# Kernel optimization log

Hardware: AMD Instinct MI355X
Metric: run time of the kernel (lower is better)

The kernel has to match this reference:

```python
import jax, jax.numpy as jnp
import numpy as np

B, Lc, Le, H, V = 128, 512, 512, 512, 128
PAD_IDX = 0  # ignore_index for cross entropy


def _lstm_cell(x, h, c, Wih, Whh, bih, bhh):
    # PyTorch gate order: i, f, g, o
    gates = x @ Wih.T + h @ Whh.T + bih + bhh
    i, f, g, o = jnp.split(gates, 4, axis=-1)
    c_new = jax.nn.sigmoid(f) * c + jax.nn.sigmoid(i) * jnp.tanh(g)
    h_new = jax.nn.sigmoid(o) * jnp.tanh(c_new)
    return h_new, c_new


def setup_inputs() -> dict:
    key = jax.random.key(0)
    ks = jax.random.split(key, 16)
    s = 0.05  # weight init scale
    inp = {
        "C": jax.random.normal(ks[0], (B, Lc, V), jnp.float32),
        "C_pad": jax.random.randint(ks[1], (B, Lc), 0, 2, jnp.int32).at[:, 0].set(0),
        "E": jax.random.randint(ks[2], (B, Le), 0, V, jnp.int32),
        "E_emb": jax.random.normal(ks[3], (B, Le, V), jnp.float32),
        # encoder LSTM (input V -> hidden H)
        "enc_Wih": s * jax.random.normal(ks[4], (4 * H, V), jnp.float32),
        "enc_Whh": s * jax.random.normal(ks[5], (4 * H, H), jnp.float32),
        "enc_bih": jnp.zeros((4 * H,), jnp.float32),
        "enc_bhh": jnp.zeros((4 * H,), jnp.float32),
        # decoder LSTMCell (input V+H -> hidden H); input is concat([E_emb_t, V_prev])
        "dec_Wih": s * jax.random.normal(ks[6], (4 * H, V + H), jnp.float32),
        "dec_Whh": s * jax.random.normal(ks[7], (4 * H, H), jnp.float32),
        "dec_bih": jnp.zeros((4 * H,), jnp.float32),
        "dec_bhh": jnp.zeros((4 * H,), jnp.float32),
        # attention_proj: Linear(H, H, bias=False)
        "att_W": s * jax.random.normal(ks[8], (H, H), jnp.float32),
        # output_proj: Linear(2H, H)
        "out_W": s * jax.random.normal(ks[9], (H, 2 * H), jnp.float32),
        "out_b": jnp.zeros((H,), jnp.float32),
        # vocab_proj: Linear(H, V)
        "voc_W": s * jax.random.normal(ks[10], (V, H), jnp.float32),
        "voc_b": jnp.zeros((V,), jnp.float32),
    }
    return inp


def reference(C, C_pad, E, E_emb, enc_Wih, enc_Whh, enc_bih, enc_bhh,
              dec_Wih, dec_Whh, dec_bih, dec_bhh, att_W, out_W, out_b,
              voc_W, voc_b):
    Bv = C.shape[0]
    Hh = enc_Whh.shape[1]

    # ---- encoder LSTM over compressed input ----
    def enc_step(carry, x_t):
        h, c = carry
        h, c = _lstm_cell(x_t, h, c, enc_Wih, enc_Whh, enc_bih, enc_bhh)
        return (h, c), h

    h0 = jnp.zeros((Bv, Hh), C.dtype)
    (hT, cT), enc_hs = jax.lax.scan(enc_step, (h0, h0), jnp.swapaxes(C, 0, 1))
    enc_hs = jnp.swapaxes(enc_hs, 0, 1)  # (B, Lc, H)
    pad = C_pad.astype(bool)              # (B, Lc)

    # ---- decoder loop (training mode, teacher forcing) ----
    def dec_step(carry, e_t):
        h, c, Vprev = carry
        x = jnp.concatenate([e_t, Vprev], axis=1)  # (B, V+H)
        h, c = _lstm_cell(x, h, c, dec_Wih, dec_Whh, dec_bih, dec_bhh)
        q = h @ att_W.T                                    # (B, H)
        scores = jnp.einsum('blh,bh->bl', enc_hs, q)       # (B, Lc)
        scores = jnp.where(pad, -jnp.inf, scores)
        d = jax.nn.softmax(scores, axis=1)
        attn = jnp.einsum('bl,blh->bh', d, enc_hs)         # (B, H)
        U = jnp.concatenate([h, attn], axis=1)             # (B, 2H)
        Vnew = U @ out_W.T + out_b                         # (B, H)
        # dropout treated as identity (eval-mode determinism)
        logits = jnp.tanh(Vnew) @ voc_W.T + voc_b          # (B, V)
        return (h, c, Vnew), logits

    Vinit = jnp.zeros((Bv, Hh), C.dtype)
    _, logits = jax.lax.scan(dec_step, (hT, cT, Vinit),
                             jnp.swapaxes(E_emb[:, :-1], 0, 1))
    logits = jnp.swapaxes(logits, 0, 1)  # (B, Le-1, V)

    # ---- cross entropy with ignore_index=PAD_IDX ----
    targets = E[:, 1:].astype(jnp.int32)
    logp = jax.nn.log_softmax(logits, axis=-1)
    nll = -jnp.take_along_axis(logp, targets[..., None], axis=-1)[..., 0]
    mask = (targets != PAD_IDX).astype(nll.dtype)
    loss = jnp.sum(nll * mask) / jnp.maximum(jnp.sum(mask), 1.0)
    return loss
```

## Files before the change

kernel.cpp:

```cpp
#include <hip/hip_runtime.h>
#include <hip/hip_bf16.h>


#define NWG 256
#define NT  256

typedef unsigned short u16;
typedef unsigned int   u32;
typedef unsigned long long u64;
typedef __attribute__((ext_vector_type(4))) float f4;
typedef __attribute__((ext_vector_type(8))) short s8;

constexpr int Bv=128, Lc=512, Le=512, Hd=512, Vc=128;
constexpr int KE=640, KD=1152;
constexpr int CAP = 144;
constexpr int SPN = 24;

constexpr size_t O_WENC = 4096;
constexpr size_t O_WDEC = O_WENC + (size_t)2048*KE*2;
constexpr size_t O_WDF  = O_WDEC + (size_t)2048*KD*2;
constexpr size_t O_ATWT = O_WDF  + (size_t)2048*KD*2;
constexpr size_t O_OUTW = O_ATWT + (size_t)512*512*2;
constexpr size_t O_VOCW = O_OUTW + (size_t)512*1024*2;
constexpr size_t O_BE   = O_VOCW + (size_t)128*512*2;
constexpr size_t O_BD   = O_BE + 8192;
constexpr size_t O_BDF  = O_BD + 8192;
constexpr size_t O_H    = O_BDF + 8192;
constexpr size_t O_TNH  = O_H + (size_t)2*128*512*2;
constexpr size_t O_PFX  = O_TNH + (size_t)2*128*512*2;
constexpr size_t O_CNT  = O_PFX + (size_t)128*512*4;
constexpr size_t O_PMS  = O_CNT + 512;
constexpr size_t O_PACC = O_PMS + 2048;
constexpr size_t O_REC  = O_PACC + (size_t)256*512*2;
constexpr size_t O_LOSS = O_REC + (size_t)2*128*2*4*4;
constexpr size_t O_ENC  = O_LOSS + 256;
constexpr size_t O_PSP  = O_ENC + (size_t)128*512*512*2;

constexpr int SC       = CAP*1024;
constexpr int SM_BYTES = SC + 16384;

struct P {
  const float *C; const int *Cpad; const int *E; const float *Eemb;
  const float *eWih,*eWhh,*ebih,*ebhh;
  const float *dWih,*dWhh,*dbih,*dbhh;
  const float *attW,*outW,*outb,*vocW,*vocb;
  char* ws; float* out;
};

__device__ inline u16 f2bf(float x){
  u32 u = __float_as_uint(x);
  return (u16)((u + 0x7fffu + ((u>>16)&1u)) >> 16);
}
__device__ inline float bf2f(u16 b){ return __uint_as_float(((u32)b)<<16); }
__device__ inline float sigm(float x){ return 1.f/(1.f+expf(-x)); }
__device__ inline f4 MM(s8 a, s8 b, f4 c){
  return __builtin_amdgcn_mfma_f32_16x16x32_bf16(a, b, c, 0, 0, 0);
}
__device__ inline u64 ld64a(const void* p){
  return __hip_atomic_load((const u64*)p, __ATOMIC_RELAXED, __HIP_MEMORY_SCOPE_AGENT);
}
__device__ inline u32 ld32u(const void* p){
  return __hip_atomic_load((const u32*)p, __ATOMIC_RELAXED, __HIP_MEMORY_SCOPE_AGENT);
}
__device__ inline void st64a(void* p, u64 v){
  __hip_atomic_store((u64*)p, v, __ATOMIC_RELAXED, __HIP_MEMORY_SCOPE_AGENT);
}
__device__ inline void st32a(void* p, u32 v){
  __hip_atomic_store((u32*)p, v, __ATOMIC_RELAXED, __HIP_MEMORY_SCOPE_AGENT);
}
__device__ inline s8 ld16a(const void* p){
  union { u64 q[2]; s8 v; } u;
  u.q[0] = ld64a(p); u.q[1] = ld64a((const char*)p + 8);
  return u.v;
}
__device__ inline s8 cvt8(const float* p){
  f4 u = *(const f4*)p, v = *(const f4*)(p+4);
  s8 r;
  r[0]=(short)f2bf(u[0]); r[1]=(short)f2bf(u[1]); r[2]=(short)f2bf(u[2]); r[3]=(short)f2bf(u[3]);
  r[4]=(short)f2bf(v[0]); r[5]=(short)f2bf(v[1]); r[6]=(short)f2bf(v[2]); r[7]=(short)f2bf(v[3]);
  return r;
}
__device__ inline float wredmax(float v){
  #pragma unroll
  for (int m=32;m;m>>=1) v = fmaxf(v, __shfl_xor(v,m,64));
  return v;
}
__device__ inline float wredsum(float v){
  #pragma unroll
  for (int m=32;m;m>>=1) v += __shfl_xor(v,m,64);
  return v;
}

extern "C" __global__ void __launch_bounds__(NT,1) k_main(P p)
{
  extern __shared__ char sm[];
  const int wg = blockIdx.x, tid = threadIdx.x;
  const int gt = wg*NT + tid;
  const int rg = wg >> 5, cg = wg & 31;

  char* ws = p.ws;
  u32*  slotA = (u32*)ws;
  u32*  slotR = (u32*)(ws + 1024 + rg*128);
  u16*  wenc = (u16*)(ws + O_WENC);
  u16*  wdec = (u16*)(ws + O_WDEC);
  u16*  wdf  = (u16*)(ws + O_WDF);
  u16*  atwt = (u16*)(ws + O_ATWT);
  u16*  outw = (u16*)(ws + O_OUTW);
  u16*  vocw = (u16*)(ws + O_VOCW);
  float* be  = (float*)(ws + O_BE);
  float* bd  = (float*)(ws + O_BD);
  float* bdf = (float*)(ws + O_BDF);
  u16*  hbf  = (u16*)(ws + O_H);
  u16*  tnhb = (u16*)(ws + O_TNH);
  u32*  pfx  = (u32*)(ws + O_PFX);
  u32*  cntp = (u32*)(ws + O_CNT);
  u64*  pms  = (u64*)(ws + O_PMS);
  u16*  pacc16 = (u16*)(ws + O_PACC);
  float* rec = (float*)(ws + O_REC);
  float* losp= (float*)(ws + O_LOSS);
  u16*  encc = (u16*)(ws + O_ENC);
  u16*  spl  = (u16*)(ws + O_PSP) + (size_t)wg*SPN*Hd;

  u32 genA = 0, genG = 0;
  auto GBall = [&](){
    genA++;
    __syncthreads();
    if (tid == 0){
      __builtin_amdgcn_fence(__ATOMIC_RELEASE, "agent");
      st32a(slotA + wg, genA);
    }
    if (tid < 64){
      bool done = false;
      while (!done){
        u32 v0 = ld32u(slotA + tid);
        u32 v1 = ld32u(slotA + 64 + tid);
        u32 v2 = ld32u(slotA + 128 + tid);
        u32 v3 = ld32u(slotA + 192 + tid);
        done = __all((v0>=genA)&&(v1>=genA)&&(v2>=genA)&&(v3>=genA));
        if (!done) __builtin_amdgcn_s_sleep(4);
      }
      __builtin_amdgcn_fence(__ATOMIC_ACQUIRE, "agent");
    }
    __syncthreads();
  };
  auto RGB = [&](){
    genG++;
    __syncthreads();
    if (tid == 0) st32a(slotR + cg, genG);
    if (tid < 64){
      bool done = false;
      while (!done){
        u32 v = ld32u(slotR + (tid & 31));
        done = __all(v >= genG);
        if (!done) __builtin_amdgcn_s_sleep(2);
      }
      __builtin_amdgcn_fence(__ATOMIC_ACQUIRE, "workgroup");
    }
    __syncthreads();
  };

  for (int i = gt; i < 2048*KE; i += NWG*NT){
    int row = i / KE, k = i - row*KE;
    float v = (k < 128) ? p.eWih[row*128 + k] : p.eWhh[row*512 + (k-128)];
    wenc[i] = f2bf(v);
  }
  for (int i = gt; i < 2048*KD; i += NWG*NT){
    int row = i / KD, k = i - row*KD;
    float v = (k < 640) ? p.dWih[row*640 + k] : p.dWhh[row*512 + (k-640)];
    wdec[i] = f2bf(v);
  }
  for (int i = gt; i < 512*512;  i += NWG*NT){
    int kk = i >> 9, j = i & 511;
    atwt[i] = f2bf(p.attW[(size_t)j*512 + kk]);
  }
  for (int i = gt; i < 512*1024; i += NWG*NT) outw[i] = f2bf(p.outW[i]);
  for (int i = gt; i < 128*512;  i += NWG*NT) vocw[i] = f2bf(p.vocW[i]);
  for (int i = gt; i < 2048;     i += NWG*NT){ be[i] = p.ebih[i]+p.ebhh[i]; bd[i] = p.dbih[i]+p.dbhh[i]; }
  { u32* hz = (u32*)hbf; for (int i = gt; i < 65536; i += NWG*NT) hz[i] = 0; }
  if (gt == 0){ losp[0] = 0.f; losp[1] = 0.f; }

  {
    const int g0 = wg*8;
    float* dv = (float*)sm;
    for (int i = tid; i < 8*512; i += NT)
      dv[i] = p.dWih[(size_t)(g0 + (i>>9))*640 + 128 + (i&511)];
    __syncthreads();
    float wa[8][4];
    #pragma unroll
    for (int r=0;r<8;r++){ wa[r][0]=0;wa[r][1]=0;wa[r][2]=0;wa[r][3]=0; }
    for (int o = 0; o < 512; o++){
      float b0 = p.outW[(size_t)o*1024 + tid];
      float b1 = p.outW[(size_t)o*1024 + 256 + tid];
      float b2 = p.outW[(size_t)o*1024 + 512 + tid];
      float b3 = p.outW[(size_t)o*1024 + 768 + tid];
      #pragma unroll
      for (int r=0;r<8;r++){
        float d = dv[r*512+o];
        wa[r][0] += d*b0; wa[r][1] += d*b1; wa[r][2] += d*b2; wa[r][3] += d*b3;
      }
    }
    #pragma unroll
    for (int r=0;r<8;r++){
      int g = g0 + r;
      #pragma unroll
      for (int j=0;j<4;j++){
        int c = tid + 256*j;
        if (c < 512) wdf[(size_t)g*KD + 128 + c] = f2bf(p.dWhh[(size_t)g*512 + c] + wa[r][j]);
        else         wdf[(size_t)g*KD + 640 + (c-512)] = f2bf(wa[r][j]);
      }
    }
    for (int i = tid; i < 8*128; i += NT){
      int r = i >> 7, k = i & 127;
      wdf[(size_t)(g0+r)*KD + k] = f2bf(p.dWih[(size_t)(g0+r)*640 + k]);
    }
    if (tid < 8){
      int g = g0 + tid;
      float s = p.dbih[g] + p.dbhh[g];
      for (int o = 0; o < 512; o++) s += dv[tid*512+o]*p.outb[o];
      bdf[g] = s;
    }
    __syncthreads();
  }

  if (wg < 128){
    int* padl = (int*)(sm + SC);
    for (int i = tid; i < 512; i += NT) padl[i] = p.Cpad[wg*512 + i];
    __syncthreads();
    if (tid == 0){
      u32 run = 0;
      for (int tt = 0; tt < 512; tt++){ pfx[wg*512+tt] = run; if (padl[tt] == 0) run++; }
      cntp[wg] = run;
    }
    __syncthreads();
  }
  GBall();

  const int l  = tid & 63, wv = tid >> 6;
  const int n2 = wv >> 1, k2 = wv & 1;
  const int kl = (l>>4) << 3;
  const int ar = rg*16 + (l&15);
  float cst = 0.f;
  float accN = 0.f, accC = 0.f;

  const int rowA = rg*16 + (cg >> 1), halfA = cg & 1;
  const int cnA = (int)cntp[rowA], c2A = cnA >> 1;
  const int loA = halfA ? c2A : 0;
  const int mynA = (halfA ? cnA : c2A) - loA;
  const int ncapA = mynA < CAP ? mynA : CAP;
  const int limA  = mynA < CAP+SPN ? mynA : CAP+SPN;
  u16* eP = (u16*)sm;

  auto CEREC = [&](int tl){
    u32* th16 = (u32*)(sm + SC + 11776);
    float* lgp = (float*)(sm + SC + 12800);
    float* lgh = (float*)(sm + SC + 13824);
    const u16* tb = tnhb + (size_t)(tl&1)*Bv*Hd + (size_t)rowA*Hd;
    th16[tid] = ld32u(tb + 2*tid);
    __syncthreads();
    {
      int v = tid & 63, ksl = tid >> 6;
      int gv = halfA*64 + v;
      const u16* wp = vocw + (size_t)gv*Hd + ksl*128;
      const u16* hp = (const u16*)th16 + ksl*128;
      float acc = 0.f;
      #pragma unroll 4
      for (int j = 0; j < 16; j++){
        s8 wv8 = *(const s8*)(wp + j*8);
        #pragma unroll
        for (int q = 0; q < 8; q++) acc += bf2f((u16)wv8[q]) * bf2f(hp[j*8+q]);
      }
      lgp[ksl*64 + v] = acc;
    }
    __syncthreads();
    if (tid < 64){
      int gv = halfA*64 + tid;
      float lv = lgp[tid] + lgp[64+tid] + lgp[128+tid] + lgp[192+tid] + p.vocb[gv];
      lgh[tid] = lv;
      float m = wredmax(lv);
      float s = wredsum(expf(lv - m));
      if (tid == 0){
        int tgt = p.E[rowA*Le + tl + 1];
        float tlg = (tgt >= halfA*64 && tgt < halfA*64+64) ? lgh[tgt - halfA*64] : 0.f;
        float* rp = rec + ((size_t)(tl&1)*256 + rowA*2 + halfA)*4;
        union { u64 q; float f[2]; } pk; pk.f[0]=m; pk.f[1]=s;
        st64a(rp, pk.q);
        st32a(rp+2, __float_as_uint(tlg));
      }
    }
    __syncthreads();
  };
  auto COMB = [&](int tl){
    int tgt = p.E[rowA*Le + tl + 1];
    if (tgt != 0){
      const float* rp = rec + ((size_t)(tl&1)*256 + rowA*2)*4;
      union { u64 q; float f[2]; } a, b;
      a.q = ld64a(rp); b.q = ld64a(rp+4);
      float tA = __uint_as_float(ld32u(rp+2)), tB = __uint_as_float(ld32u(rp+6));
      float M = fmaxf(a.f[0], b.f[0]);
      float S = a.f[1]*expf(a.f[0]-M) + b.f[1]*expf(b.f[0]-M);
      accN += logf(S) + M - (tA + tB);
      accC += 1.f;
    }
  };

  const int gR0 = (n2*2+0)*512 + cg*16 + (l&15);
  const int gR1 = (n2*2+1)*512 + cg*16 + (l&15);

  for (int t = 0; t < Lc; t++){
    const u16* hold = hbf + (t&1)*Bv*Hd;
    u16* hnew       = hbf + ((t+1)&1)*Bv*Hd;
    s8 a[10];
    #pragma unroll
    for (int ks = 0; ks < 10; ks++){
      int k = k2*320 + ks*32 + kl;
      if (k < 128) a[ks] = cvt8(p.C + ((size_t)ar*Lc + t)*Vc + k);
      else         a[ks] = ld16a(hold + (size_t)ar*Hd + (k-128));
    }
    f4 acc0 = {0,0,0,0}, acc1 = {0,0,0,0};
    #pragma unroll
    for (int ks = 0; ks < 10; ks++){
      int k = k2*320 + ks*32 + kl;
      acc0 = MM(a[ks], *(const s8*)(wenc + (size_t)gR0*KE + k), acc0);
      acc1 = MM(a[ks], *(const s8*)(wenc + (size_t)gR1*KE + k), acc1);
    }
    float* exch = (float*)(sm + SC);
    #pragma unroll
    for (int r = 0; r < 4; r++){
      int row = ((l>>4)<<2) + r;
      exch[((k2*4 + n2*2+0)*16 + row)*16 + (l&15)] = acc0[r];
      exch[((k2*4 + n2*2+1)*16 + row)*16 + (l&15)] = acc1[r];
    }
    __syncthreads();
    {
      int row = tid >> 4, u = tid & 15;
      int gb = cg*16 + u;
      float gi = exch[((0)*16+row)*16+u] + exch[((4)*16+row)*16+u] + be[0*512+gb];
      float gf = exch[((1)*16+row)*16+u] + exch[((5)*16+row)*16+u] + be[1*512+gb];
      float gg = exch[((2)*16+row)*16+u] + exch[((6)*16+row)*16+u] + be[2*512+gb];
      float go = exch[((3)*16+row)*16+u] + exch[((7)*16+row)*16+u] + be[3*512+gb];
      float fi = sigm(gi), ff = sigm(gf), fg = tanhf(gg), fo = sigm(go);
      cst = ff*cst + fi*fg;
      float hn = fo * tanhf(cst);
      int b = rg*16 + row;
      u32 hb = f2bf(hn);
      u32 nb = __shfl_xor((int)hb, 1, 64);
      if ((tid & 1) == 0){
        u32 pk = hb | (nb << 16);
        st32a(hnew + (size_t)b*Hd + gb, pk);
        if (p.Cpad[b*Lc + t] == 0){
          u32 pos = pfx[b*Lc + t];
          st32a(encc + ((size_t)b*Lc + pos)*Hd + gb, pk);
        }
      }
    }
    RGB();
  }

  GBall();

  {
    const u16* erow = encc + ((size_t)rowA*Lc + loA)*Hd;
    for (int it = 0; it*16 < limA; it++){
      s8 afr[16];
      const u16* ap = erow + (size_t)(it*16 + (l&15))*Hd;
      #pragma unroll
      for (int ks = 0; ks < 16; ks++) afr[ks] = *(const s8*)(ap + ks*32 + kl);
      for (int ot = 0; ot < 8; ot++){
        int kout0 = wv*128 + ot*16;
        f4 acc = {0,0,0,0};
        #pragma unroll
        for (int ks = 0; ks < 16; ks++)
          acc = MM(afr[ks], *(const s8*)(atwt + (size_t)(kout0 + (l&15))*Hd + ks*32 + kl), acc);
        #pragma unroll
        for (int r = 0; r < 4; r++){
          int prow = it*16 + ((l>>4)<<2) + r;
          int pcol = kout0 + (l&15);
          if (prow < limA){
            u16 pv = f2bf(acc[r]);
            if (prow < CAP) eP[(size_t)prow*Hd + pcol] = pv;
            else            spl[(size_t)(prow-CAP)*Hd + pcol] = pv;
          }
        }
      }
    }
    __syncthreads();
  }

  float* exch = (float*)(sm + SC);
  float* vex  = (float*)(sm + SC + 8192);
  float* sc2  = (float*)(sm + SC + 12288);
  s8 aH[14];

  for (int t = 0; t < Le-1; t++){
    const u16* hold = hbf + (t&1)*Bv*Hd;
    u16* hnew       = hbf + ((t+1)&1)*Bv*Hd;

    if (t == 0){
      s8 a[10];
      #pragma unroll
      for (int ks = 0; ks < 10; ks++){
        int ke = (k2==0) ? ((ks<4) ? ks*32+kl : 640 + (ks-4)*32 + kl)
                         : (832 + ks*32 + kl);
        if (ke < 128) a[ks] = cvt8(p.Eemb + ((size_t)ar*Le + 0)*Vc + ke);
        else          a[ks] = ld16a(hold + (size_t)ar*Hd + (ke-640));
      }
      f4 acc0 = {0,0,0,0}, acc1 = {0,0,0,0};
      #pragma unroll
      for (int ks = 0; ks < 10; ks++){
        int ke = (k2==0) ? ((ks<4) ? ks*32+kl : 640 + (ks-4)*32 + kl)
                         : (832 + ks*32 + kl);
        acc0 = MM(a[ks], *(const s8*)(wdec + (size_t)gR0*KD + ke), acc0);
        acc1 = MM(a[ks], *(const s8*)(wdec + (size_t)gR1*KD + ke), acc1);
      }
      #pragma unroll
      for (int r = 0; r < 4; r++){
        int row = ((l>>4)<<2) + r;
        exch[((k2*4 + n2*2+0)*16 + row)*16 + (l&15)] = acc0[r];
        exch[((k2*4 + n2*2+1)*16 + row)*16 + (l&15)] = acc1[r];
      }
      __syncthreads();
      {
        int row = tid >> 4, u = tid & 15;
        int gb = cg*16 + u;
        float gi = exch[((0)*16+row)*16+u] + exch[((4)*16+row)*16+u] + bd[0*512+gb];
        float gf = exch[((1)*16+row)*16+u] + exch[((5)*16+row)*16+u] + bd[1*512+gb];
        float gg = exch[((2)*16+row)*16+u] + exch[((6)*16+row)*16+u] + bd[2*512+gb];
        float go = exch[((3)*16+row)*16+u] + exch[((7)*16+row)*16+u] + bd[3*512+gb];
        float fi = sigm(gi), ff = sigm(gf), fg = tanhf(gg), fo = sigm(go);
        cst = ff*cst + fi*fg;
        float hn = fo * tanhf(cst);
        u32 hb = f2bf(hn);
        u32 nb = __shfl_xor((int)hb, 1, 64);
        if ((tid & 1) == 0)
          st32a(hnew + (size_t)(rg*16+row)*Hd + gb, hb | (nb << 16));
      }
    } else {
      if (tid < 16){
        union { u64 q; float f[2]; } uA, uB;
        uA.q = ld64a(pms + (rg*16+tid)*2 + 0);
        uB.q = ld64a(pms + (rg*16+tid)*2 + 1);
        float M = fmaxf(uA.f[0], uB.f[0]);
        float eA = (uA.f[0] > -1e29f) ? expf(uA.f[0]-M) : 0.f;
        float eB = (uB.f[0] > -1e29f) ? expf(uB.f[0]-M) : 0.f;
        float den = uA.f[1]*eA + uB.f[1]*eB;
        sc2[tid*2]   = eA/den;
        sc2[tid*2+1] = eB/den;
      }
      __syncthreads();
      const float scA = sc2[(l&15)*2], scB = sc2[(l&15)*2+1];
      const u16* pA = pacc16 + (size_t)(ar*2+0)*Hd;
      const u16* pB = pacc16 + (size_t)(ar*2+1)*Hd;
      s8 a[18];
      if (k2 == 0){
        #pragma unroll
        for (int ks = 0; ks < 4; ks++)
          a[ks] = cvt8(p.Eemb + ((size_t)ar*Le + t)*Vc + ks*32 + kl);
        #pragma unroll
        for (int ks = 4; ks < 18; ks++) a[ks] = aH[ks-4];
      } else {
        a[0] = aH[0]; a[1] = aH[1];
        #pragma unroll
        for (int ks = 2; ks < 18; ks++){
          int k = 576 + ks*32 + kl;
          s8 va = ld16a(pA + (k-640));
          s8 vb = ld16a(pB + (k-640));
          s8 r;
          #pragma unroll
          for (int j = 0; j < 8; j++)
            r[j] = (short)f2bf(scA*bf2f((u16)va[j]) + scB*bf2f((u16)vb[j]));
          a[ks] = r;
        }
      }
      f4 acc0 = {0,0,0,0}, acc1 = {0,0,0,0};
      #pragma unroll
      for (int ks = 0; ks < 18; ks++){
        int k = k2*576 + ks*32 + kl;
        acc0 = MM(a[ks], *(const s8*)(wdf + (size_t)gR0*KD + k), acc0);
        acc1 = MM(a[ks], *(const s8*)(wdf + (size_t)gR1*KD + k), acc1);
      }
      f4 vac = {0,0,0,0};
      const int colc = cg*16 + (l&15);
      #pragma unroll
      for (int ks = 0; ks < 18; ks++){
        int ck = k2*18 + ks - 4;
        if (ck >= 0 && ((ck & 1) == n2))
          vac = MM(a[ks], *(const s8*)(outw + (size_t)colc*1024 + ck*32 + kl), vac);
      }
      #pragma unroll
      for (int r = 0; r < 4; r++){
        int row = ((l>>4)<<2) + r;
        exch[((k2*4 + n2*2+0)*16 + row)*16 + (l&15)] = acc0[r];
        exch[((k2*4 + n2*2+1)*16 + row)*16 + (l&15)] = acc1[r];
        vex[wv*256 + row*16 + (l&15)] = vac[r];
      }
      __syncthreads();
      {
        int row = tid >> 4, u = tid & 15;
        int gb = cg*16 + u;
        float gi = exch[((0)*16+row)*16+u] + exch[((4)*16+row)*16+u] + bdf[0*512+gb];
        float gf = exch[((1)*16+row)*16+u] + exch[((5)*16+row)*16+u] + bdf[1*512+gb];
        float gg = exch[((2)*16+row)*16+u] + exch[((6)*16+row)*16+u] + bdf[2*512+gb];
        float go = exch[((3)*16+row)*16+u] + exch[((7)*16+row)*16+u] + bdf[3*512+gb];
        float fi = sigm(gi), ff = sigm(gf), fg = tanhf(gg), fo = sigm(go);
        cst = ff*cst + fi*fg;
        float hn = fo * tanhf(cst);
        u32 hb = f2bf(hn);
        u32 nb = __shfl_xor((int)hb, 1, 64);
        if ((tid & 1) == 0)
          st32a(hnew + (size_t)(rg*16+row)*Hd + gb, hb | (nb << 16));
        float v = vex[row*16+u] + vex[256+row*16+u] + vex[512+row*16+u]
                + vex[768+row*16+u] + p.outb[gb];
        u32 tb2 = f2bf(tanhf(v));
        u32 tn2 = __shfl_xor((int)tb2, 1, 64);
        if ((tid & 1) == 0){
          u16* tnw = tnhb + (size_t)((t-1)&1)*Bv*Hd;
          st32a(tnw + (size_t)(rg*16+row)*Hd + gb, tb2 | (tn2 << 16));
        }
      }
    }
    RGB();

    {
      const int ne = limA, ncap = ncapA;
      float* hld = (float*)(sm + SC);
      float* scl = (float*)(sm + SC + 2048);
      float* red = (float*)(sm + SC + 2816);
      float* part= (float*)(sm + SC + 3584);
      {
        u32 hw = ld32u(hnew + (size_t)rowA*Hd + 2*tid);
        int c0 = 2*tid, c1 = c0+1;
        hld[(c0&15)*32 + (c0>>4)] = bf2f((u16)(hw & 0xffffu));
        hld[(c1&15)*32 + (c1>>4)] = bf2f((u16)(hw >> 16));
      }
      __syncthreads();
      const int pg8 = tid >> 5, ln = tid & 31;
      int i = pg8;
      for (; i < ncap; i += 8){
        const u16* e = eP + (size_t)i*Hd + ln*16;
        s8 ev0 = *(const s8*)(e);
        s8 ev1 = *(const s8*)(e+8);
        float s = 0.f;
        #pragma unroll
        for (int j=0;j<8;j++) s += bf2f((u16)ev0[j]) * hld[j*32+ln];
        #pragma unroll
        for (int j=0;j<8;j++) s += bf2f((u16)ev1[j]) * hld[(j+8)*32+ln];
        #pragma unroll
        for (int m=1;m<32;m<<=1) s += __shfl_xor(s, m, 64);
        if (ln == 0) scl[i] = s;
      }
      for (; i < ne; i += 8){
        const u16* e = spl + (size_t)(i-CAP)*Hd + ln*16;
        s8 ev0 = *(const s8*)(e);
        s8 ev1 = *(const s8*)(e+8);
        float s = 0.f;
        #pragma unroll
        for (int j=0;j<8;j++) s += bf2f((u16)ev0[j]) * hld[j*32+ln];
        #pragma unroll
        for (int j=0;j<8;j++) s += bf2f((u16)ev1[j]) * hld[(j+8)*32+ln];
        #pragma unroll
        for (int m=1;m<32;m<<=1) s += __shfl_xor(s, m, 64);
        if (ln == 0) scl[i] = s;
      }
      __syncthreads();
      float mloc = -1e30f;
      for (int i2 = tid; i2 < ne; i2 += NT) mloc = fmaxf(mloc, scl[i2]);
      mloc = wredmax(mloc);
      if ((tid&63)==0) red[tid>>6] = mloc;
      __syncthreads();
      float M = fmaxf(fmaxf(red[0],red[1]), fmaxf(red[2],red[3]));
      __syncthreads();
      float sloc = 0.f;
      for (int i2 = tid; i2 < ne; i2 += NT){ float w = expf(scl[i2]-M); scl[i2]=w; sloc += w; }
      sloc = wredsum(sloc);
      if ((tid&63)==0) red[tid>>6] = sloc;
      __syncthreads();
      float S = red[0]+red[1]+red[2]+red[3];
      float a8[8] = {0,0,0,0,0,0,0,0};
      const u16* eb2 = encc + ((size_t)rowA*Lc + loA)*Hd + l*8;
      int ii = wv;
      for (; ii + 12 < ne; ii += 16){
        s8 e0 = *(const s8*)(eb2 + (size_t)(ii   )*Hd);
        s8 e1 = *(const s8*)(eb2 + (size_t)(ii+ 4)*Hd);
        s8 e2 = *(const s8*)(eb2 + (size_t)(ii+ 8)*Hd);
        s8 e3 = *(const s8*)(eb2 + (size_t)(ii+12)*Hd);
        float w0=scl[ii], w1=scl[ii+4], w2=scl[ii+8], w3=scl[ii+12];
        #pragma unroll
        for (int j=0;j<8;j++) a8[j] += w0*bf2f((u16)e0[j]);
        #pragma unroll
        for (int j=0;j<8;j++) a8[j] += w1*bf2f((u16)e1[j]);
        #pragma unroll
        for (int j=0;j<8;j++) a8[j] += w2*bf2f((u16)e2[j]);
        #pragma unroll
        for (int j=0;j<8;j++) a8[j] += w3*bf2f((u16)e3[j]);
      }
      for (; ii < ne; ii += 4){
        s8 e0 = *(const s8*)(eb2 + (size_t)ii*Hd);
        float w0 = scl[ii];
        #pragma unroll
        for (int j=0;j<8;j++) a8[j] += w0*bf2f((u16)e0[j]);
      }
      { f4 v0 = {a8[0],a8[1],a8[2],a8[3]}, v1 = {a8[4],a8[5],a8[6],a8[7]};
        *(f4*)(part + wv*512 + l*8)     = v0;
        *(f4*)(part + wv*512 + l*8 + 4) = v1; }
      __syncthreads();
      {
        int h0 = 2*tid;
        float a0 = part[h0] + part[512+h0] + part[1024+h0] + part[1536+h0];
        float a1 = part[h0+1] + part[512+h0+1] + part[1024+h0+1] + part[1536+h0+1];
        st32a(pacc16 + (size_t)(rowA*2+halfA)*Hd + h0, (u32)f2bf(a0) | ((u32)f2bf(a1) << 16));
        if (tid == 0){
          union { u64 q; float f[2]; } pk; pk.f[0]=M; pk.f[1]=S;
          st64a(pms + rowA*2 + halfA, pk.q);
        }
      }
      __syncthreads();
      if (t >= 1) CEREC(t-1);
      if (t >= 2 && halfA == 0 && tid == 0) COMB(t-2);
      if (t < Le-2){
        if (k2 == 0){
          #pragma unroll
          for (int ks = 4; ks < 18; ks++)
            aH[ks-4] = ld16a(hnew + (size_t)ar*Hd + (ks*32 + kl - 128));
        } else {
          aH[0] = ld16a(hnew + (size_t)ar*Hd + (448 + kl));
          aH[1] = ld16a(hnew + (size_t)ar*Hd + (480 + kl));
        }
      }
    }
    RGB();
  }

  const int TL = Le-2;
  {
    if (tid < 16){
      union { u64 q; float f[2]; } uA, uB;
      uA.q = ld64a(pms + (rg*16+tid)*2 + 0);
      uB.q = ld64a(pms + (rg*16+tid)*2 + 1);
      float M = fmaxf(uA.f[0], uB.f[0]);
      float eA = (uA.f[0] > -1e29f) ? expf(uA.f[0]-M) : 0.f;
      float eB = (uB.f[0] > -1e29f) ? expf(uB.f[0]-M) : 0.f;
      float den = uA.f[1]*eA + uB.f[1]*eB;
      sc2[tid*2]   = eA/den;
      sc2[tid*2+1] = eB/den;
    }
    __syncthreads();
    const float scA = sc2[(l&15)*2], scB = sc2[(l&15)*2+1];
    const u16* h5 = hbf + (size_t)((TL+1)&1)*Bv*Hd;
    const u16* pA = pacc16 + (size_t)(ar*2+0)*Hd;
    const u16* pB = pacc16 + (size_t)(ar*2+1)*Hd;
    const int colc = cg*16 + (l&15);
    f4 vac = {0,0,0,0};
    #pragma unroll
    for (int j = 0; j < 8; j++){
      int kv = k2*16 + j*2 + n2;
      s8 af;
      if (kv < 16) af = ld16a(h5 + (size_t)ar*Hd + kv*32 + kl);
      else {
        s8 va = ld16a(pA + (kv-16)*32 + kl);
        s8 vb = ld16a(pB + (kv-16)*32 + kl);
        #pragma unroll
        for (int q = 0; q < 8; q++)
          af[q] = (short)f2bf(scA*bf2f((u16)va[q]) + scB*bf2f((u16)vb[q]));
      }
      vac = MM(af, *(const s8*)(outw + (size_t)colc*1024 + kv*32 + kl), vac);
    }
    #pragma unroll
    for (int r = 0; r < 4; r++)
      vex[wv*256 + (((l>>4)<<2)+r)*16 + (l&15)] = vac[r];
    __syncthreads();
    {
      int row = tid >> 4, u = tid & 15;
      int gb = cg*16 + u;
      float v = vex[row*16+u] + vex[256+row*16+u] + vex[512+row*16+u]
              + vex[768+row*16+u] + p.outb[gb];
      u32 tb2 = f2bf(tanhf(v));
      u32 tn2 = __shfl_xor((int)tb2, 1, 64);
      if ((tid & 1) == 0){
        u16* tnw = tnhb + (size_t)(TL&1)*Bv*Hd;
        st32a(tnw + (size_t)(rg*16+row)*Hd + gb, tb2 | (tn2 << 16));
      }
    }
  }
  RGB();
  {
    CEREC(TL);
    if (halfA == 0 && tid == 0) COMB(TL-1);
  }
  RGB();
  {
    if (halfA == 0 && tid == 0){
      COMB(TL);
      atomicAdd(losp + 0, accN);
      atomicAdd(losp + 1, accC);
    }
  }
  GBall();
  if (wg == 0 && tid == 0) p.out[0] = losp[0] / fmaxf(losp[1], 1.f);
}

extern "C" void kernel_launch(void* const* d_in, const int* in_sizes, int n_in,
                              void* d_out, int out_size, void* d_ws, size_t ws_size,
                              hipStream_t stream)
{
  hipFuncSetAttribute(reinterpret_cast<const void*>(k_main),
                      hipFuncAttributeMaxDynamicSharedMemorySize, SM_BYTES);
  hipMemsetAsync(d_ws, 0, 4096, stream);

  P prm;
  prm.C    = (const float*)d_in[0];
  prm.Cpad = (const int*)  d_in[1];
  prm.E    = (const int*)  d_in[2];
  prm.Eemb = (const float*)d_in[3];
  prm.eWih = (const float*)d_in[4];
  prm.eWhh = (const float*)d_in[5];
  prm.ebih = (const float*)d_in[6];
  prm.ebhh = (const float*)d_in[7];
  prm.dWih = (const float*)d_in[8];
  prm.dWhh = (const float*)d_in[9];
  prm.dbih = (const float*)d_in[10];
  prm.dbhh = (const float*)d_in[11];
  prm.attW = (const float*)d_in[12];
  prm.outW = (const float*)d_in[13];
  prm.outb = (const float*)d_in[14];
  prm.vocW = (const float*)d_in[15];
  prm.vocb = (const float*)d_in[16];
  prm.ws   = (char*)d_ws;
  prm.out  = (float*)d_out;

  k_main<<<dim3(NWG), dim3(NT), SM_BYTES, stream>>>(prm);
}
```

Measured before the change: 21.30 ms.

## Apply attention softmax weights after the MFMA instead of scaling partial accumulators first

In the decoder step, the k2==1 waves no longer blend the two partial attention accumulators into a bf16 operand before the matrix multiply. Each partial runs through the MFMA separately and the result is scaled by its softmax weight per output row. This removes the per-element bf16 convert/scale/convert work on the critical path, but doubles the MFMA count for the attention part. The encoder's operand loads are also split by k2 to remove the per-element branch, and the gate and vocab MFMAs are interleaved in one loop.

```diff
diff --git a/kernel.cpp b/kernel.cpp
--- a/kernel.cpp
+++ b/kernel.cpp
@@ -310,11 +310,17 @@
     const u16* hold = hbf + (t&1)*Bv*Hd;
     u16* hnew       = hbf + ((t+1)&1)*Bv*Hd;
     s8 a[10];
-    #pragma unroll
-    for (int ks = 0; ks < 10; ks++){
-      int k = k2*320 + ks*32 + kl;
-      if (k < 128) a[ks] = cvt8(p.C + ((size_t)ar*Lc + t)*Vc + k);
-      else         a[ks] = ld16a(hold + (size_t)ar*Hd + (k-128));
+    if (k2 == 0){
+      #pragma unroll
+      for (int ks = 4; ks < 10; ks++)
+        a[ks] = ld16a(hold + (size_t)ar*Hd + (ks*32 + kl - 128));
+      #pragma unroll
+      for (int ks = 0; ks < 4; ks++)
+        a[ks] = cvt8(p.C + ((size_t)ar*Lc + t)*Vc + ks*32 + kl);
+    } else {
+      #pragma unroll
+      for (int ks = 0; ks < 10; ks++)
+        a[ks] = ld16a(hold + (size_t)ar*Hd + (192 + ks*32 + kl));
     }
     f4 acc0 = {0,0,0,0}, acc1 = {0,0,0,0};
     #pragma unroll
@@ -447,51 +453,86 @@
         sc2[tid*2+1] = eB/den;
       }
       __syncthreads();
-      const float scA = sc2[(l&15)*2], scB = sc2[(l&15)*2+1];
-      const u16* pA = pacc16 + (size_t)(ar*2+0)*Hd;
-      const u16* pB = pacc16 + (size_t)(ar*2+1)*Hd;
-      s8 a[18];
+      const int colc = cg*16 + (l&15);
       if (k2 == 0){
+        s8 a[18];
+        #pragma unroll
+        for (int ks = 4; ks < 18; ks++) a[ks] = aH[ks-4];
         #pragma unroll
         for (int ks = 0; ks < 4; ks++)
           a[ks] = cvt8(p.Eemb + ((size_t)ar*Le + t)*Vc + ks*32 + kl);
-        #pragma unroll
-        for (int ks = 4; ks < 18; ks++) a[ks] = aH[ks-4];
+        f4 acc0 = {0,0,0,0}, acc1 = {0,0,0,0}, vac = {0,0,0,0};
+        #pragma unroll
+        for (int ks = 0; ks < 18; ks++){
+          int k = ks*32 + kl;
+          acc0 = MM(a[ks], *(const s8*)(wdf + (size_t)gR0*KD + k), acc0);
+          acc1 = MM(a[ks], *(const s8*)(wdf + (size_t)gR1*KD + k), acc1);
+          int ck = ks - 4;
+          if (ck >= 0 && ((ck & 1) == n2))
+            vac = MM(a[ks], *(const s8*)(outw + (size_t)colc*1024 + ck*32 + kl), vac);
+        }
+        #pragma unroll
+        for (int r = 0; r < 4; r++){
+          int row = ((l>>4)<<2) + r;
+          exch[((n2*2+0)*16 + row)*16 + (l&15)] = acc0[r];
+          exch[((n2*2+1)*16 + row)*16 + (l&15)] = acc1[r];
+          vex[wv*256 + row*16 + (l&15)] = vac[r];
+        }
       } else {
-        a[0] = aH[0]; a[1] = aH[1];
-        #pragma unroll
-        for (int ks = 2; ks < 18; ks++){
-          int k = 576 + ks*32 + kl;
-          s8 va = ld16a(pA + (k-640));
-          s8 vb = ld16a(pB + (k-640));
-          s8 r;
+        const u16* pA = pacc16 + (size_t)(ar*2+0)*Hd;
+        const u16* pB = pacc16 + (size_t)(ar*2+1)*Hd;
+        s8 h0f = aH[0], h1f = aH[1];
+        f4 acc0 = {0,0,0,0}, acc1 = {0,0,0,0};
+        f4 aA0 = {0,0,0,0}, aA1 = {0,0,0,0}, aB0 = {0,0,0,0}, aB1 = {0,0,0,0};
+        f4 vH = {0,0,0,0}, vA = {0,0,0,0}, vB = {0,0,0,0};
+        acc0 = MM(h0f, *(const s8*)(wdf + (size_t)gR0*KD + 576 + kl), acc0);
+        acc1 = MM(h0f, *(const s8*)(wdf + (size_t)gR1*KD + 576 + kl), acc1);
+        acc0 = MM(h1f, *(const s8*)(wdf + (size_t)gR0*KD + 608 + kl), acc0);
+        acc1 = MM(h1f, *(const s8*)(wdf + (size_t)gR1*KD + 608 + kl), acc1);
+        {
+          s8 hf = (n2 == 0) ? h0f : h1f;
+          vH = MM(hf, *(const s8*)(outw + (size_t)colc*1024 + (14+n2)*32 + kl), vH);
+        }
+        #pragma unroll
+        for (int hb = 0; hb < 2; hb++){
+          s8 pf[8];
           #pragma unroll
           for (int j = 0; j < 8; j++)
-            r[j] = (short)f2bf(scA*bf2f((u16)va[j]) + scB*bf2f((u16)vb[j]));
-          a[ks] = r;
-        }
-      }
-      f4 acc0 = {0,0,0,0}, acc1 = {0,0,0,0};
-      #pragma unroll
-      for (int ks = 0; ks < 18; ks++){
-        int k = k2*576 + ks*32 + kl;
-        acc0 = MM(a[ks], *(const s8*)(wdf + (size_t)gR0*KD + k), acc0);
-        acc1 = MM(a[ks], *(const s8*)(wdf + (size_t)gR1*KD + k), acc1);
-      }
-      f4 vac = {0,0,0,0};
-      const int colc = cg*16 + (l&15);
-      #pragma unroll
-      for (int ks = 0; ks < 18; ks++){
-        int ck = k2*18 + ks - 4;
-        if (ck >= 0 && ((ck & 1) == n2))
-          vac = MM(a[ks], *(const s8*)(outw + (size_t)colc*1024 + ck*32 + kl), vac);
-      }
-      #pragma unroll
-      for (int r = 0; r < 4; r++){
-        int row = ((l>>4)<<2) + r;
-        exch[((k2*4 + n2*2+0)*16 + row)*16 + (l&15)] = acc0[r];
-        exch[((k2*4 + n2*2+1)*16 + row)*16 + (l&15)] = acc1[r];
-        vex[wv*256 + row*16 + (l&15)] = vac[r];
+            pf[j] = ld16a(pA + (hb*8+j)*32 + kl);
+          #pragma unroll
+          for (int j = 0; j < 8; j++){
+            int c = hb*8 + j;
+            int k = 640 + c*32 + kl;
+            aA0 = MM(pf[j], *(const s8*)(wdf + (size_t)gR0*KD + k), aA0);
+            aA1 = MM(pf[j], *(const s8*)(wdf + (size_t)gR1*KD + k), aA1);
+            if (((16 + c) & 1) == n2)
+              vA = MM(pf[j], *(const s8*)(outw + (size_t)colc*1024 + (16+c)*32 + kl), vA);
+          }
+        }
+        #pragma unroll
+        for (int hb = 0; hb < 2; hb++){
+          s8 pf[8];
+          #pragma unroll
+          for (int j = 0; j < 8; j++)
+            pf[j] = ld16a(pB + (hb*8+j)*32 + kl);
+          #pragma unroll
+          for (int j = 0; j < 8; j++){
+            int c = hb*8 + j;
+            int k = 640 + c*32 + kl;
+            aB0 = MM(pf[j], *(const s8*)(wdf + (size_t)gR0*KD + k), aB0);
+            aB1 = MM(pf[j], *(const s8*)(wdf + (size_t)gR1*KD + k), aB1);
+            if (((16 + c) & 1) == n2)
+              vB = MM(pf[j], *(const s8*)(outw + (size_t)colc*1024 + (16+c)*32 + kl), vB);
+          }
+        }
+        #pragma unroll
+        for (int r = 0; r < 4; r++){
+          int row = ((l>>4)<<2) + r;
+          float sAr = sc2[row*2], sBr = sc2[row*2+1];
+          exch[((4 + n2*2+0)*16 + row)*16 + (l&15)] = acc0[r] + sAr*aA0[r] + sBr*aB0[r];
+          exch[((4 + n2*2+1)*16 + row)*16 + (l&15)] = acc1[r] + sAr*aA1[r] + sBr*aB1[r];
+          vex[wv*256 + row*16 + (l&15)] = vH[r] + sAr*vA[r] + sBr*vB[r];
+        }
       }
       __syncthreads();
       {
```

New measurement: 21.57 ms. No clear change (+1.2%).
